# Optimization experiments

Measured on AMD Instinct MI355X. Metric: run time of the kernel, lower is better.

Reference implementation:

```python
import jax, jax.numpy as jnp
import numpy as np

N_HEAD, D_MODEL, D_K, D_V = 8, 512, 64, 64
LN_EPS = 1e-3


def setup_inputs() -> dict:
    key = jax.random.key(0)
    ks = jax.random.split(key, 9)
    B, L = 4, 2048
    q = jax.random.normal(ks[0], (B, L, D_MODEL), dtype=jnp.float32)
    k = jax.random.normal(ks[1], (B, L, D_MODEL), dtype=jnp.float32)
    v = jax.random.normal(ks[2], (B, L, D_MODEL), dtype=jnp.float32)
    # xavier-normal-ish init for projections
    s_qk = (2.0 / (D_MODEL + D_K)) ** 0.5
    s_v = (2.0 / (D_MODEL + D_V)) ** 0.5
    s_p = (2.0 / (N_HEAD * D_V + D_MODEL)) ** 0.5
    w_qs = jax.random.normal(ks[3], (N_HEAD, D_MODEL, D_K), dtype=jnp.float32) * s_qk
    w_ks = jax.random.normal(ks[4], (N_HEAD, D_MODEL, D_K), dtype=jnp.float32) * s_qk
    w_vs = jax.random.normal(ks[5], (N_HEAD, D_MODEL, D_V), dtype=jnp.float32) * s_v
    proj_w = jax.random.normal(ks[6], (D_MODEL, N_HEAD * D_V), dtype=jnp.float32) * s_p  # torch Linear weight (out,in)
    proj_b = jnp.zeros((D_MODEL,), dtype=jnp.float32)
    a_2 = jnp.ones((D_MODEL,), dtype=jnp.float32)
    b_2 = jnp.zeros((D_MODEL,), dtype=jnp.float32)
    return {"q": q, "k": k, "v": v, "w_qs": w_qs, "w_ks": w_ks, "w_vs": w_vs,
            "proj_w": proj_w, "proj_b": proj_b, "a_2": a_2, "b_2": b_2}


def _layer_norm(z, a_2, b_2):
    # torch.std default is unbiased (ddof=1); module divides by (sigma + eps)
    mu = jnp.mean(z, axis=-1, keepdims=True)
    sigma = jnp.std(z, axis=-1, keepdims=True, ddof=1)
    return (z - mu) / (sigma + LN_EPS) * a_2 + b_2


def reference(q, k, v, w_qs, w_ks, w_vs, proj_w, proj_b, a_2, b_2):
    B, Lq, D = q.shape
    temper = jnp.asarray(D, q.dtype) ** 0.5  # note: sqrt(d_model), as in source
    residual = q
    # per-head projections: (h, b, l, dk)
    qh = jnp.einsum('bld,hdk->hblk', q, w_qs)
    kh = jnp.einsum('bmd,hdk->hbmk', k, w_ks)
    vh = jnp.einsum('bmd,hdv->hbmv', v, w_vs)
    # full score matrix (h, b, lq, lk) -- faithful to naive bmm attention
    attn = jax.nn.softmax(jnp.einsum('hblk,hbmk->hblm', qh, kh) / temper, axis=-1)
    out = jnp.einsum('hblm,hbmv->hblv', attn, vh)          # (h, b, lq, dv)
    out = jnp.transpose(out, (1, 2, 0, 3)).reshape(B, Lq, -1)  # concat heads -> (b, lq, h*dv)
    out = out @ proj_w.T + proj_b
    out = _layer_norm(out + residual, a_2, b_2)
    attns = attn.reshape(-1, attn.shape[2], attn.shape[3])  # (h*b, lq, lk) matching torch layout
    return out, attns
```

## Files before the change

### kernel.cpp

```cpp
#include <hip/hip_runtime.h>
#include <stdint.h>

typedef unsigned short u16;
typedef u16   u16x4v __attribute__((ext_vector_type(4)));
typedef u16   u16x8v __attribute__((ext_vector_type(8)));
typedef short s16x8v __attribute__((ext_vector_type(8)));
typedef float f32x4v __attribute__((ext_vector_type(4)));

#define DEV static __device__ __forceinline__

DEV u16 f2bf(float f){
  union { float f; unsigned u; } v; v.f = f;
  unsigned r = v.u + 0x7FFFu + ((v.u >> 16) & 1u);
  return (u16)(r >> 16);
}

DEV f32x4v mfma16(s16x8v a, s16x8v b, f32x4v c){
  return __builtin_amdgcn_mfma_f32_16x16x32_bf16(a, b, c, 0, 0, 0);
}

__global__ __launch_bounds__(256) void k_wall(const float* __restrict__ w_qs,
                                              const float* __restrict__ w_ks,
                                              const float* __restrict__ w_vs,
                                              const float* __restrict__ proj_w,
                                              u16* __restrict__ wt, u16* __restrict__ wtp,
                                              float qscale){
  int gid = blockIdx.x;
  int tsel = gid >> 10;
  int e = (gid & 1023) * 256 + threadIdx.x;
  if(tsel == 3){
    wtp[e] = f2bf(proj_w[e]);
  } else {
    const float* w = tsel == 0 ? w_qs : (tsel == 1 ? w_ks : w_vs);
    float sc = tsel == 0 ? qscale : 1.0f;
    int n = e >> 9, d = e & 511;
    int h = n >> 6, kk = n & 63;
    wt[tsel * 262144 + n * 512 + d] = f2bf(w[h * 32768 + d * 64 + kk] * sc);
  }
}

__global__ __launch_bounds__(256) void k_qkv(const float* __restrict__ Q,
                                             const float* __restrict__ K,
                                             const float* __restrict__ V,
                                             const u16* __restrict__ Wt,
                                             u16* __restrict__ qhh, u16* __restrict__ khh,
                                             u16* __restrict__ vtt){
  __shared__ __align__(16) u16 Xs[32 * 520];
  const int t = threadIdx.x;
  const int lane = t & 63, w = t >> 6;
  const int g = lane >> 4, li = lane & 15;
  const int i0 = blockIdx.x * 32;
  const int y = blockIdx.y;
  const int tsel = y >> 1;
  const float* X = tsel == 0 ? Q : (tsel == 1 ? K : V);
  const int n0 = (y & 1) * 256 + w * 64;

  #pragma unroll
  for(int it = 0; it < 16; ++it){
    int s = it * 256 + t, row = s >> 7, c4 = s & 127;
    f32x4v xv = *(const f32x4v*)(X + (size_t)(i0 + row) * 512 + c4 * 4);
    u16x4v bv; bv[0]=f2bf(xv[0]); bv[1]=f2bf(xv[1]); bv[2]=f2bf(xv[2]); bv[3]=f2bf(xv[3]);
    *(u16x4v*)(Xs + row * 520 + c4 * 4) = bv;
  }
  __syncthreads();

  const int wbase = tsel * 512 + n0;
  const u16* wp0 = Wt + (size_t)(wbase +  0 + li) * 512 + g * 8;
  const u16* wp1 = Wt + (size_t)(wbase + 16 + li) * 512 + g * 8;
  const u16* wp2 = Wt + (size_t)(wbase + 32 + li) * 512 + g * 8;
  const u16* wp3 = Wt + (size_t)(wbase + 48 + li) * 512 + g * 8;

#define LOADW(S, c) { \
  S##0 = *(const s16x8v*)(wp0 + (c) * 32); \
  S##1 = *(const s16x8v*)(wp1 + (c) * 32); \
  S##2 = *(const s16x8v*)(wp2 + (c) * 32); \
  S##3 = *(const s16x8v*)(wp3 + (c) * 32); }
#define COMPW(S, c) { \
  int k0 = (c) * 32 + g * 8; \
  s16x8v a0 = *(const s16x8v*)(Xs + li * 520 + k0); \
  s16x8v a1 = *(const s16x8v*)(Xs + (16 + li) * 520 + k0); \
  acc[0][0] = mfma16(a0, S##0, acc[0][0]); acc[1][0] = mfma16(a1, S##0, acc[1][0]); \
  acc[0][1] = mfma16(a0, S##1, acc[0][1]); acc[1][1] = mfma16(a1, S##1, acc[1][1]); \
  acc[0][2] = mfma16(a0, S##2, acc[0][2]); acc[1][2] = mfma16(a1, S##2, acc[1][2]); \
  acc[0][3] = mfma16(a0, S##3, acc[0][3]); acc[1][3] = mfma16(a1, S##3, acc[1][3]); }

  f32x4v acc[2][4] = {};
  s16x8v wA0, wA1, wA2, wA3, wB0, wB1, wB2, wB3;
  LOADW(wA, 0);
  #pragma unroll
  for(int c = 0; c < 16; c += 2){
    LOADW(wB, c + 1);
    COMPW(wA, c);
    if(c + 2 < 16) LOADW(wA, c + 2);
    COMPW(wB, c + 1);
  }
#undef LOADW
#undef COMPW

  if(tsel < 2){
    u16* Y = tsel == 0 ? qhh : khh;
    #pragma unroll
    for(int rg = 0; rg < 2; ++rg)
      #pragma unroll
      for(int j = 0; j < 4; ++j){
        int n = n0 + j * 16 + li, h = n >> 6, dk = n & 63;
        #pragma unroll
        for(int r = 0; r < 4; ++r){
          int i = i0 + rg * 16 + g * 4 + r, bb = i >> 11, m = i & 2047;
          Y[((size_t)(h * 4 + bb) * 2048 + m) * 64 + dk] = f2bf(acc[rg][j][r]);
        }
      }
  } else {
    #pragma unroll
    for(int rg = 0; rg < 2; ++rg)
      #pragma unroll
      for(int j = 0; j < 4; ++j){
        int n = n0 + j * 16 + li;
        u16x4v pk;
        #pragma unroll
        for(int r = 0; r < 4; ++r) pk[r] = f2bf(acc[rg][j][r]);
        *(u16x4v*)(vtt + (size_t)n * 8192 + i0 + g * 8 + rg * 4) = pk;
      }
  }
}


#define LOADK(B, ht) { \
  const u16* _p = kp + (size_t)(ht) * 2048; \
  B##0 = *(const s16x8v*)(_p); \
  B##1 = *(const s16x8v*)(_p + 32); \
  B##2 = *(const s16x8v*)(_p + 1024); \
  B##3 = *(const s16x8v*)(_p + 1056); }

#define STEPA(B) { \
  f32x4v z0 = {}, z1 = {}; \
  z0 = mfma16(B##0, bq00, z0); z0 = mfma16(B##1, bq01, z0); \
  z1 = mfma16(B##2, bq00, z1); z1 = mfma16(B##3, bq01, z1); \
  _Pragma("unroll") for(int r = 0; r < 4; ++r){ s00[r] += exp2f(z0[r]); s01[r] += exp2f(z1[r]); } \
  f32x4v y0 = {}, y1 = {}; \
  y0 = mfma16(B##0, bq10, y0); y0 = mfma16(B##1, bq11, y0); \
  y1 = mfma16(B##2, bq10, y1); y1 = mfma16(B##3, bq11, y1); \
  _Pragma("unroll") for(int r = 0; r < 4; ++r){ s10[r] += exp2f(y0[r]); s11[r] += exp2f(y1[r]); } }

#define LOADV(B, ht) { \
  const u16* _p = vp + (ht) * 32; \
  B##0 = *(const s16x8v*)(_p); \
  B##1 = *(const s16x8v*)(_p + 131072); \
  B##2 = *(const s16x8v*)(_p + 262144); \
  B##3 = *(const s16x8v*)(_p + 393216); }

#define QS_HALF(KB, VB, bqa, bqb, rl, qs, ht) { \
  f32x4v z0 = {}, z1 = {}; \
  z0 = mfma16(KB##0, bqa, z0); z0 = mfma16(KB##1, bqb, z0); \
  z1 = mfma16(KB##2, bqa, z1); z1 = mfma16(KB##3, bqb, z1); \
  f32x4v p0, p1; \
  _Pragma("unroll") for(int r = 0; r < 4; ++r){ p0[r] = exp2f(z0[r]) * rl; p1[r] = exp2f(z1[r]) * rl; } \
  float* _ab = attb + (size_t)((qs) * 16 + li) * 2048 + (ht) * 32 + g * 4; \
  __builtin_nontemporal_store(p0, (f32x4v*)(_ab)); \
  __builtin_nontemporal_store(p1, (f32x4v*)(_ab + 16)); \
  union { u16 hh[8]; s16x8v v; } _u; \
  _Pragma("unroll") for(int r = 0; r < 4; ++r){ _u.hh[r] = f2bf(p0[r]); _u.hh[4 + r] = f2bf(p1[r]); } \
  acc##qs##0 = mfma16(_u.v, VB##0, acc##qs##0); \
  acc##qs##1 = mfma16(_u.v, VB##1, acc##qs##1); \
  acc##qs##2 = mfma16(_u.v, VB##2, acc##qs##2); \
  acc##qs##3 = mfma16(_u.v, VB##3, acc##qs##3); }

#define STEPB(KB, VB, ht) { \
  QS_HALF(KB, VB, bq00, bq01, rl0, 0, ht); \
  QS_HALF(KB, VB, bq10, bq11, rl1, 1, ht); }

__global__ __launch_bounds__(256) void k_attn(const u16* __restrict__ QHH, const u16* __restrict__ KHH,
                                              const u16* __restrict__ VTT,
                                              u16* __restrict__ XC, float* __restrict__ ATT){
  const int t = threadIdx.x, lane = t & 63, w = t >> 6;
  const int g = lane >> 4, li = lane & 15;
  const int gid = blockIdx.x;
  const int xcd = gid & 7, rem = gid >> 3;
  const int lt = rem & 15;
  const int hb = xcd * 4 + (rem >> 4);
  const int h = hb >> 2, b = hb & 3;
  const size_t base_hb = (size_t)hb * 2048;
  const int qbase = lt * 128 + w * 32;

  s16x8v bq00, bq01, bq10, bq11;
  {
    const u16* qp0 = QHH + (base_hb + qbase + li) * 64 + g * 8;
    const u16* qp1 = QHH + (base_hb + qbase + 16 + li) * 64 + g * 8;
    bq00 = *(const s16x8v*)(qp0); bq01 = *(const s16x8v*)(qp0 + 32);
    bq10 = *(const s16x8v*)(qp1); bq11 = *(const s16x8v*)(qp1 + 32);
  }
  const u16* kp = KHH + (base_hb + li) * 64 + g * 8;
  const u16* vp = VTT + (size_t)(h * 64 + li) * 8192 + b * 2048 + g * 8;

  f32x4v s00 = {}, s01 = {}, s10 = {}, s11 = {};
  {
    s16x8v kA0, kA1, kA2, kA3, kB0, kB1, kB2, kB3;
    LOADK(kA, 0);
    for(int ht = 0; ht < 62; ht += 2){
      LOADK(kB, ht + 1);
      STEPA(kA);
      LOADK(kA, ht + 2);
      STEPA(kB);
    }
    LOADK(kB, 63);
    STEPA(kA);
    STEPA(kB);
  }
  float l0 = (s00[0]+s00[1]+s00[2]+s00[3]) + (s01[0]+s01[1]+s01[2]+s01[3]);
  float l1 = (s10[0]+s10[1]+s10[2]+s10[3]) + (s11[0]+s11[1]+s11[2]+s11[3]);
  l0 += __shfl_xor(l0, 16, 64); l0 += __shfl_xor(l0, 32, 64);
  l1 += __shfl_xor(l1, 16, 64); l1 += __shfl_xor(l1, 32, 64);
  const float rl0 = 1.0f / l0;
  const float rl1 = 1.0f / l1;

  float* attb = ATT + (base_hb + qbase) * 2048;
  f32x4v acc00 = {}, acc01 = {}, acc02 = {}, acc03 = {};
  f32x4v acc10 = {}, acc11 = {}, acc12 = {}, acc13 = {};
  {
    s16x8v kA0, kA1, kA2, kA3, kB0, kB1, kB2, kB3;
    s16x8v vA0, vA1, vA2, vA3, vB0, vB1, vB2, vB3;
    LOADK(kA, 0); LOADV(vA, 0);
    for(int ht = 0; ht < 62; ht += 2){
      LOADK(kB, ht + 1); LOADV(vB, ht + 1);
      STEPB(kA, vA, ht);
      LOADK(kA, ht + 2); LOADV(vA, ht + 2);
      STEPB(kB, vB, ht + 1);
    }
    LOADK(kB, 63); LOADV(vB, 63);
    STEPB(kA, vA, 62);
    STEPB(kB, vB, 63);
  }

  #pragma unroll
  for(int r = 0; r < 4; ++r){
    int row0 = qbase + g * 4 + r;
    int row1 = qbase + 16 + g * 4 + r;
    u16* x0 = XC + (size_t)(b * 2048 + row0) * 512 + h * 64 + li;
    u16* x1 = XC + (size_t)(b * 2048 + row1) * 512 + h * 64 + li;
    x0[0]  = f2bf(acc00[r]); x0[16] = f2bf(acc01[r]); x0[32] = f2bf(acc02[r]); x0[48] = f2bf(acc03[r]);
    x1[0]  = f2bf(acc10[r]); x1[16] = f2bf(acc11[r]); x1[32] = f2bf(acc12[r]); x1[48] = f2bf(acc13[r]);
  }
}

__global__ __launch_bounds__(512) void k_out(const u16* __restrict__ Xb,
                                             const u16* __restrict__ Wtp,
                                             float* __restrict__ Yf,
                                             const float* __restrict__ bias,
                                             const float* __restrict__ resid,
                                             const float* __restrict__ a2,
                                             const float* __restrict__ b2){
  __shared__ __align__(16) u16 Xs[16 * 520];
  __shared__ float sred[8][16], sqred[8][16], muL[16], rsL[16];
  const int t = threadIdx.x;
  const int lane = t & 63, w = t >> 6;
  const int g = lane >> 4, li = lane & 15;
  const int i0 = blockIdx.x * 16;
  const int n0 = w * 64;

  #pragma unroll
  for(int it = 0; it < 2; ++it){
    int s = it * 512 + t, row = s >> 6, c8 = s & 63;
    u16x8v xv = *(const u16x8v*)(Xb + (size_t)(i0 + row) * 512 + c8 * 8);
    *(u16x8v*)(Xs + row * 520 + c8 * 8) = xv;
  }
  __syncthreads();

  const u16* wp0 = Wtp + (size_t)(n0 +  0 + li) * 512 + g * 8;
  const u16* wp1 = Wtp + (size_t)(n0 + 16 + li) * 512 + g * 8;
  const u16* wp2 = Wtp + (size_t)(n0 + 32 + li) * 512 + g * 8;
  const u16* wp3 = Wtp + (size_t)(n0 + 48 + li) * 512 + g * 8;

#define LOADW(S, c) { \
  S##0 = *(const s16x8v*)(wp0 + (c) * 32); \
  S##1 = *(const s16x8v*)(wp1 + (c) * 32); \
  S##2 = *(const s16x8v*)(wp2 + (c) * 32); \
  S##3 = *(const s16x8v*)(wp3 + (c) * 32); }
#define COMPW(S, c) { \
  int k0 = (c) * 32 + g * 8; \
  s16x8v a0 = *(const s16x8v*)(Xs + li * 520 + k0); \
  acc[0] = mfma16(a0, S##0, acc[0]); \
  acc[1] = mfma16(a0, S##1, acc[1]); \
  acc[2] = mfma16(a0, S##2, acc[2]); \
  acc[3] = mfma16(a0, S##3, acc[3]); }

  f32x4v acc[4] = {};
  s16x8v wA0, wA1, wA2, wA3, wB0, wB1, wB2, wB3;
  LOADW(wA, 0);
  #pragma unroll
  for(int c = 0; c < 16; c += 2){
    LOADW(wB, c + 1);
    COMPW(wA, c);
    if(c + 2 < 16) LOADW(wA, c + 2);
    COMPW(wB, c + 1);
  }
#undef LOADW
#undef COMPW

  float zres[4][4];
  #pragma unroll
  for(int j = 0; j < 4; ++j){
    int n = n0 + j * 16 + li;
    float bv = bias[n];
    #pragma unroll
    for(int r = 0; r < 4; ++r){
      int i = i0 + g * 4 + r;
      zres[j][r] = acc[j][r] + bv + resid[(size_t)i * 512 + n];
    }
  }
  #pragma unroll
  for(int r = 0; r < 4; ++r){
    float S = 0.f, SQ = 0.f;
    #pragma unroll
    for(int j = 0; j < 4; ++j){ float zz = zres[j][r]; S += zz; SQ += zz * zz; }
    #pragma unroll
    for(int off = 1; off < 16; off <<= 1){ S += __shfl_xor(S, off, 16); SQ += __shfl_xor(SQ, off, 16); }
    if(li == 0){ sred[w][g * 4 + r] = S; sqred[w][g * 4 + r] = SQ; }
  }
  __syncthreads();
  if(t < 16){
    float S = 0.f, SQ = 0.f;
    #pragma unroll
    for(int ww = 0; ww < 8; ++ww){ S += sred[ww][t]; SQ += sqred[ww][t]; }
    float mu = S * (1.0f / 512.0f);
    float var = (SQ - 512.0f * mu * mu) * (1.0f / 511.0f);
    muL[t] = mu;
    rsL[t] = 1.0f / (sqrtf(fmaxf(var, 0.0f)) + 1e-3f);
  }
  __syncthreads();
  #pragma unroll
  for(int r = 0; r < 4; ++r){
    int rloc = g * 4 + r;
    float mu = muL[rloc], rs = rsL[rloc];
    size_t ib = (size_t)(i0 + rloc) * 512;
    #pragma unroll
    for(int j = 0; j < 4; ++j){
      int n = n0 + j * 16 + li;
      Yf[ib + n] = (zres[j][r] - mu) * rs * a2[n] + b2[n];
    }
  }
}

extern "C" void kernel_launch(void* const* d_in, const int* in_sizes, int n_in,
                              void* d_out, int out_size, void* d_ws, size_t ws_size,
                              hipStream_t stream){
  const float* q      = (const float*)d_in[0];
  const float* k      = (const float*)d_in[1];
  const float* v      = (const float*)d_in[2];
  const float* w_qs   = (const float*)d_in[3];
  const float* w_ks   = (const float*)d_in[4];
  const float* w_vs   = (const float*)d_in[5];
  const float* proj_w = (const float*)d_in[6];
  const float* proj_b = (const float*)d_in[7];
  const float* a2     = (const float*)d_in[8];
  const float* b2     = (const float*)d_in[9];

  char* ws = (char*)d_ws;
  u16* wt    = (u16*)(ws);
  u16* wtp   = (u16*)(ws + 1572864);
  u16* qhh   = (u16*)(ws + 2097152);
  u16* khh   = (u16*)(ws + 10485760);
  u16* vtt   = (u16*)(ws + 18874368);
  u16* xc    = (u16*)(ws + 27262976);

  float* out = (float*)d_out;
  float* att = out + 4194304;

  const float qscale = 0.06375872032774575f;

  k_wall<<<dim3(4096), 256, 0, stream>>>(w_qs, w_ks, w_vs, proj_w, wt, wtp, qscale);
  k_qkv <<<dim3(256, 6), 256, 0, stream>>>(q, k, v, wt, qhh, khh, vtt);
  k_attn<<<dim3(512), 256, 0, stream>>>(qhh, khh, vtt, xc, att);
  k_out <<<dim3(512), 512, 0, stream>>>(xc, wtp, out, proj_b, q, a2, b2);
}
```

Baseline: 318.7 us.

## Split attention key dimension across wave pairs with LDS reduction of row sums and outputs

Each block now covers 64 query rows instead of 128, and two waves share each 32-row query slice, each handling half of the 2048 keys. Partial softmax denominators are combined through shared memory before normalization, and the partial PV accumulators are summed in LDS before the bf16 output is written. The grid doubles to 1024 blocks, the V register double-buffer is dropped to cut register use, and launch bounds request 4 blocks per CU for higher occupancy. This adds two block barriers and an LDS reduction step.

```diff
diff --git a/kernel.cpp b/kernel.cpp
--- a/kernel.cpp
+++ b/kernel.cpp
@@ -142,45 +142,48 @@
   y1 = mfma16(B##2, bq10, y1); y1 = mfma16(B##3, bq11, y1); \
   _Pragma("unroll") for(int r = 0; r < 4; ++r){ s10[r] += exp2f(y0[r]); s11[r] += exp2f(y1[r]); } }
 
-#define LOADV(B, ht) { \
+#define LOADV(ht) { \
   const u16* _p = vp + (ht) * 32; \
-  B##0 = *(const s16x8v*)(_p); \
-  B##1 = *(const s16x8v*)(_p + 131072); \
-  B##2 = *(const s16x8v*)(_p + 262144); \
-  B##3 = *(const s16x8v*)(_p + 393216); }
-
-#define QS_HALF(KB, VB, bqa, bqb, rl, qs, ht) { \
+  vA0 = *(const s16x8v*)(_p); \
+  vA1 = *(const s16x8v*)(_p + 131072); \
+  vA2 = *(const s16x8v*)(_p + 262144); \
+  vA3 = *(const s16x8v*)(_p + 393216); }
+
+#define QS_HALF(KB, bqa, bqb, rl, qs_, ht) { \
   f32x4v z0 = {}, z1 = {}; \
   z0 = mfma16(KB##0, bqa, z0); z0 = mfma16(KB##1, bqb, z0); \
   z1 = mfma16(KB##2, bqa, z1); z1 = mfma16(KB##3, bqb, z1); \
   f32x4v p0, p1; \
   _Pragma("unroll") for(int r = 0; r < 4; ++r){ p0[r] = exp2f(z0[r]) * rl; p1[r] = exp2f(z1[r]) * rl; } \
-  float* _ab = attb + (size_t)((qs) * 16 + li) * 2048 + (ht) * 32 + g * 4; \
+  float* _ab = attb + (size_t)((qs_) * 16 + li) * 2048 + (ht) * 32 + g * 4; \
   __builtin_nontemporal_store(p0, (f32x4v*)(_ab)); \
   __builtin_nontemporal_store(p1, (f32x4v*)(_ab + 16)); \
   union { u16 hh[8]; s16x8v v; } _u; \
   _Pragma("unroll") for(int r = 0; r < 4; ++r){ _u.hh[r] = f2bf(p0[r]); _u.hh[4 + r] = f2bf(p1[r]); } \
-  acc##qs##0 = mfma16(_u.v, VB##0, acc##qs##0); \
-  acc##qs##1 = mfma16(_u.v, VB##1, acc##qs##1); \
-  acc##qs##2 = mfma16(_u.v, VB##2, acc##qs##2); \
-  acc##qs##3 = mfma16(_u.v, VB##3, acc##qs##3); }
-
-#define STEPB(KB, VB, ht) { \
-  QS_HALF(KB, VB, bq00, bq01, rl0, 0, ht); \
-  QS_HALF(KB, VB, bq10, bq11, rl1, 1, ht); }
-
-__global__ __launch_bounds__(256) void k_attn(const u16* __restrict__ QHH, const u16* __restrict__ KHH,
-                                              const u16* __restrict__ VTT,
-                                              u16* __restrict__ XC, float* __restrict__ ATT){
+  acc##qs_##0 = mfma16(_u.v, vA0, acc##qs_##0); \
+  acc##qs_##1 = mfma16(_u.v, vA1, acc##qs_##1); \
+  acc##qs_##2 = mfma16(_u.v, vA2, acc##qs_##2); \
+  acc##qs_##3 = mfma16(_u.v, vA3, acc##qs_##3); }
+
+#define STEPB(KB, ht) { \
+  QS_HALF(KB, bq00, bq01, rl0, 0, ht); \
+  QS_HALF(KB, bq10, bq11, rl1, 1, ht); }
+
+__global__ __launch_bounds__(256, 4) void k_attn(const u16* __restrict__ QHH, const u16* __restrict__ KHH,
+                                                 const u16* __restrict__ VTT,
+                                                 u16* __restrict__ XC, float* __restrict__ ATT){
+  __shared__ float Lp[2][2][32];
+  __shared__ float AccS[2][32][64];
   const int t = threadIdx.x, lane = t & 63, w = t >> 6;
   const int g = lane >> 4, li = lane & 15;
+  const int qs = w >> 1, mh = w & 1;
   const int gid = blockIdx.x;
   const int xcd = gid & 7, rem = gid >> 3;
-  const int lt = rem & 15;
-  const int hb = xcd * 4 + (rem >> 4);
+  const int qt = rem & 31;
+  const int hb = xcd * 4 + (rem >> 5);
   const int h = hb >> 2, b = hb & 3;
   const size_t base_hb = (size_t)hb * 2048;
-  const int qbase = lt * 128 + w * 32;
+  const int qbase = qt * 64 + qs * 32;
 
   s16x8v bq00, bq01, bq10, bq11;
   {
@@ -189,20 +192,21 @@
     bq00 = *(const s16x8v*)(qp0); bq01 = *(const s16x8v*)(qp0 + 32);
     bq10 = *(const s16x8v*)(qp1); bq11 = *(const s16x8v*)(qp1 + 32);
   }
-  const u16* kp = KHH + (base_hb + li) * 64 + g * 8;
-  const u16* vp = VTT + (size_t)(h * 64 + li) * 8192 + b * 2048 + g * 8;
+  const u16* kp = KHH + (base_hb + li) * 64 + g * 8 + (size_t)mh * 65536;
+  const u16* vp = VTT + (size_t)(h * 64 + li) * 8192 + b * 2048 + g * 8 + mh * 1024;
+  float* attb = ATT + (base_hb + qbase) * 2048 + mh * 1024;
 
   f32x4v s00 = {}, s01 = {}, s10 = {}, s11 = {};
   {
     s16x8v kA0, kA1, kA2, kA3, kB0, kB1, kB2, kB3;
     LOADK(kA, 0);
-    for(int ht = 0; ht < 62; ht += 2){
+    for(int ht = 0; ht < 30; ht += 2){
       LOADK(kB, ht + 1);
       STEPA(kA);
       LOADK(kA, ht + 2);
       STEPA(kB);
     }
-    LOADK(kB, 63);
+    LOADK(kB, 31);
     STEPA(kA);
     STEPA(kB);
   }
@@ -210,35 +214,64 @@
   float l1 = (s10[0]+s10[1]+s10[2]+s10[3]) + (s11[0]+s11[1]+s11[2]+s11[3]);
   l0 += __shfl_xor(l0, 16, 64); l0 += __shfl_xor(l0, 32, 64);
   l1 += __shfl_xor(l1, 16, 64); l1 += __shfl_xor(l1, 32, 64);
-  const float rl0 = 1.0f / l0;
-  const float rl1 = 1.0f / l1;
-
-  float* attb = ATT + (base_hb + qbase) * 2048;
+  if(lane < 16){ Lp[qs][mh][li] = l0; Lp[qs][mh][16 + li] = l1; }
+  __syncthreads();
+  const float rl0 = 1.0f / (Lp[qs][0][li]      + Lp[qs][1][li]);
+  const float rl1 = 1.0f / (Lp[qs][0][16 + li] + Lp[qs][1][16 + li]);
+
   f32x4v acc00 = {}, acc01 = {}, acc02 = {}, acc03 = {};
   f32x4v acc10 = {}, acc11 = {}, acc12 = {}, acc13 = {};
   {
     s16x8v kA0, kA1, kA2, kA3, kB0, kB1, kB2, kB3;
-    s16x8v vA0, vA1, vA2, vA3, vB0, vB1, vB2, vB3;
-    LOADK(kA, 0); LOADV(vA, 0);
-    for(int ht = 0; ht < 62; ht += 2){
-      LOADK(kB, ht + 1); LOADV(vB, ht + 1);
-      STEPB(kA, vA, ht);
-      LOADK(kA, ht + 2); LOADV(vA, ht + 2);
-      STEPB(kB, vB, ht + 1);
-    }
-    LOADK(kB, 63); LOADV(vB, 63);
-    STEPB(kA, vA, 62);
-    STEPB(kB, vB, 63);
-  }
-
-  #pragma unroll
-  for(int r = 0; r < 4; ++r){
-    int row0 = qbase + g * 4 + r;
-    int row1 = qbase + 16 + g * 4 + r;
-    u16* x0 = XC + (size_t)(b * 2048 + row0) * 512 + h * 64 + li;
-    u16* x1 = XC + (size_t)(b * 2048 + row1) * 512 + h * 64 + li;
-    x0[0]  = f2bf(acc00[r]); x0[16] = f2bf(acc01[r]); x0[32] = f2bf(acc02[r]); x0[48] = f2bf(acc03[r]);
-    x1[0]  = f2bf(acc10[r]); x1[16] = f2bf(acc11[r]); x1[32] = f2bf(acc12[r]); x1[48] = f2bf(acc13[r]);
+    s16x8v vA0, vA1, vA2, vA3;
+    LOADK(kA, 0);
+    for(int ht = 0; ht < 30; ht += 2){
+      LOADK(kB, ht + 1); LOADV(ht);
+      STEPB(kA, ht);
+      LOADK(kA, ht + 2); LOADV(ht + 1);
+      STEPB(kB, ht + 1);
+    }
+    LOADK(kB, 31); LOADV(30);
+    STEPB(kA, 30);
+    LOADV(31);
+    STEPB(kB, 31);
+  }
+
+  if(mh == 1){
+    #pragma unroll
+    for(int r = 0; r < 4; ++r){
+      AccS[qs][ 0 + r][lane] = acc00[r];
+      AccS[qs][ 4 + r][lane] = acc01[r];
+      AccS[qs][ 8 + r][lane] = acc02[r];
+      AccS[qs][12 + r][lane] = acc03[r];
+      AccS[qs][16 + r][lane] = acc10[r];
+      AccS[qs][20 + r][lane] = acc11[r];
+      AccS[qs][24 + r][lane] = acc12[r];
+      AccS[qs][28 + r][lane] = acc13[r];
+    }
+  }
+  __syncthreads();
+  if(mh == 0){
+    #pragma unroll
+    for(int r = 0; r < 4; ++r){
+      acc00[r] += AccS[qs][ 0 + r][lane];
+      acc01[r] += AccS[qs][ 4 + r][lane];
+      acc02[r] += AccS[qs][ 8 + r][lane];
+      acc03[r] += AccS[qs][12 + r][lane];
+      acc10[r] += AccS[qs][16 + r][lane];
+      acc11[r] += AccS[qs][20 + r][lane];
+      acc12[r] += AccS[qs][24 + r][lane];
+      acc13[r] += AccS[qs][28 + r][lane];
+    }
+    #pragma unroll
+    for(int r = 0; r < 4; ++r){
+      int row0 = qbase + g * 4 + r;
+      int row1 = qbase + 16 + g * 4 + r;
+      u16* x0 = XC + (size_t)(b * 2048 + row0) * 512 + h * 64 + li;
+      u16* x1 = XC + (size_t)(b * 2048 + row1) * 512 + h * 64 + li;
+      x0[0]  = f2bf(acc00[r]); x0[16] = f2bf(acc01[r]); x0[32] = f2bf(acc02[r]); x0[48] = f2bf(acc03[r]);
+      x1[0]  = f2bf(acc10[r]); x1[16] = f2bf(acc11[r]); x1[32] = f2bf(acc12[r]); x1[48] = f2bf(acc13[r]);
+    }
   }
 }
 
@@ -369,6 +402,6 @@
 
   k_wall<<<dim3(4096), 256, 0, stream>>>(w_qs, w_ks, w_vs, proj_w, wt, wtp, qscale);
   k_qkv <<<dim3(256, 6), 256, 0, stream>>>(q, k, v, wt, qhh, khh, vtt);
-  k_attn<<<dim3(512), 256, 0, stream>>>(qhh, khh, vtt, xc, att);
+  k_attn<<<dim3(1024), 256, 0, stream>>>(qhh, khh, vtt, xc, att);
   k_out <<<dim3(512), 512, 0, stream>>>(xc, wtp, out, proj_b, q, a2, b2);
 }
```

New measurement: 314.1 us. Within noise of the previous version (-1.5%).
